# Performance work log

Measured on AMD Instinct MI355X. Metric: run time of the kernel, lower is better.

Reference implementation:

```python
import jax, jax.numpy as jnp
import numpy as np

BEV = 100  # fixed 100x100 BEV grid from __init__


def _bev_grids():
    # x: arange(-25+0.125, 25, 0.5) -> 100 vals; z: arange(0.125, 50, 0.5) -> 100 vals
    x = jnp.arange(-25.0 + 0.125, 25.0, 0.5, dtype=jnp.float32)
    z = jnp.arange(0.125, 50.0, 0.5, dtype=jnp.float32)
    zz, xx = jnp.meshgrid(z, x, indexing='ij')           # [100,100]
    xz = xx / zz                                          # [100,100]
    yz = jnp.stack([-1.0 / zz, 0.5 / zz, 2.0 / zz], 0)    # [3,100,100], planes y=-1,0.5,2
    return xz, yz


def _grid_sample_bilinear(img, grid):
    """torch.nn.functional.grid_sample, mode='bilinear', padding_mode='zeros',
    align_corners=False. img [B,C,H,W], grid [B,Hg,Wg,2] in [-1,1] (u=x, v=y)."""
    B, C, H, W = img.shape
    x = ((grid[..., 0] + 1.0) * W - 1.0) * 0.5            # unnormalized pixel x
    y = ((grid[..., 1] + 1.0) * H - 1.0) * 0.5
    x0f = jnp.floor(x)
    y0f = jnp.floor(y)
    x0 = x0f.astype(jnp.int32)
    y0 = y0f.astype(jnp.int32)
    x1 = x0 + 1
    y1 = y0 + 1
    wx1 = x - x0f
    wx0 = 1.0 - wx1
    wy1 = y - y0f
    wy0 = 1.0 - wy1

    def corner(xi, yi, w):
        valid = ((xi >= 0) & (xi < W) & (yi >= 0) & (yi < H)).astype(img.dtype)
        xi_c = jnp.clip(xi, 0, W - 1)
        yi_c = jnp.clip(yi, 0, H - 1)
        # per-batch gather: [C,H,W] indexed by [Hg,Wg] -> [C,Hg,Wg]
        vals = jax.vmap(lambda im, yy, xx_: im[:, yy, xx_])(img, yi_c, xi_c)
        return vals * (w * valid)[:, None]                 # [B,C,Hg,Wg]

    return (corner(x0, y0, wx0 * wy0) + corner(x1, y0, wx1 * wy0)
            + corner(x0, y1, wx0 * wy1) + corner(x1, y1, wx1 * wy1))


def setup_inputs() -> dict:
    key = jax.random.key(0)
    k1, k2, k3, k4, k5 = jax.random.split(key, 5)
    B, C, H, W = 8, 512, 88, 176
    img_w, img_h = 704, 352
    img_feature = jax.random.normal(k1, (B, C, H, W), dtype=jnp.float32)
    # realistic pinhole intrinsics so many BEV cells project in-bounds
    fx = jax.random.uniform(k2, (B,), minval=450.0, maxval=650.0)
    fy = jax.random.uniform(k3, (B,), minval=450.0, maxval=650.0)
    cx = img_w / 2.0 + jax.random.uniform(k4, (B,), minval=-8.0, maxval=8.0)
    cy = img_h / 2.0 + jax.random.uniform(k5, (B,), minval=-8.0, maxval=8.0)
    intrinsic = (jnp.zeros((B, 3, 3), dtype=jnp.float32)
                 .at[:, 0, 0].set(fx).at[:, 1, 1].set(fy)
                 .at[:, 0, 2].set(cx).at[:, 1, 2].set(cy)
                 .at[:, 2, 2].set(1.0))
    return {"img_feature": img_feature, "intrinsic": intrinsic,
            "img_w": img_w, "img_h": img_h}


def reference(img_feature, intrinsic, img_w, img_h):
    xz, yz = _bev_grids()
    fx = intrinsic[:, 0, 0][:, None, None]
    cx = intrinsic[:, 0, 2][:, None, None]
    fy = intrinsic[:, 1, 1][:, None, None]
    cy = intrinsic[:, 1, 2][:, None, None]
    u = ((fx * xz[None] + cx) / img_w - 0.5) * 2.0        # [B,100,100], shared by all 3 planes
    acc = None
    for k in range(3):                                     # 3 fixed height planes
        v = ((fy * yz[k][None] + cy) / img_h - 0.5) * 2.0
        grid = jnp.stack((u, v), axis=3)                   # [B,100,100,2]
        s = _grid_sample_bilinear(img_feature, grid)       # [B,C,100,100]
        acc = s if acc is None else acc + s
    return acc / 3.0
```

## Files before the change

kernel.cpp:

```cpp
#include <hip/hip_runtime.h>

#define BEVN 100
#define NB 8
#define NC 512
#define FH 88
#define FW 176
#define HWSZ (FH * FW)
#define NG4  (HWSZ / 4)
#define G4PR (FW / 4)
#define NPAIR (BEVN * BEVN / 2)

typedef float    f32x4 __attribute__((ext_vector_type(4)));
typedef float    f32x2 __attribute__((ext_vector_type(2)));
typedef unsigned u32x4 __attribute__((ext_vector_type(4)));

__device__ __forceinline__ unsigned bf16rne(float f) {
    const unsigned b = __float_as_uint(f);
    return (b + 0x7fffu + ((b >> 16) & 1u)) >> 16;
}
__device__ __forceinline__ float lo16f(unsigned u) { return __uint_as_float(u << 16); }
__device__ __forceinline__ float hi16f(unsigned u) { return __uint_as_float(u & 0xffff0000u); }

__global__ __launch_bounds__(1024, 8)
void vt_kernel(const float* __restrict__ img,
               const float* __restrict__ intr,
               const int* __restrict__ p_imw,
               const int* __restrict__ p_imh,
               float* __restrict__ out)
{
    __shared__ unsigned      buf[HWSZ];
    __shared__ float4        ytab[BEVN * 3];
    __shared__ unsigned char marked[FH];

    const int blk = blockIdx.x;
    const int b   = blk >> 8;
    const int bc0 = b * NC + (blk & 255) * 2;
    const int tid = (int)threadIdx.x;

    const float fx  = intr[b * 9 + 0];
    const float cxv = intr[b * 9 + 2];
    const float fy  = intr[b * 9 + 4];
    const float cyv = intr[b * 9 + 5];
    const float wsc = (float)FW / (float)p_imw[0];
    const float hsc = (float)FH / (float)p_imh[0];

    if (tid < FH) marked[tid] = 0;
    __syncthreads();

    if (tid < BEVN * 3) {
        const int   i  = tid / 3;
        const int   k  = tid - 3 * i;
        const float z  = 0.125f + 0.5f * (float)i;
        const float iz = 1.0f / z;
        const float yk = (k == 0) ? -1.0f : ((k == 1) ? 0.5f : 2.0f);
        const float yp = fmaf(fy * yk * iz + cyv, hsc, -0.5f);
        const float yf = floorf(yp);
        const int   y0 = (int)yf;
        float wy1 = yp - yf;
        float wy0 = 1.0f - wy1;
        wy0 = ((unsigned)y0 < (unsigned)FH) ? wy0 : 0.0f;
        wy1 = ((unsigned)(y0 + 1) < (unsigned)FH) ? wy1 : 0.0f;
        if (wy0 != 0.0f) marked[y0] = 1;
        if (wy1 != 0.0f) marked[y0 + 1] = 1;
        const int yb0 = min(max(y0, 0), FH - 1) * FW;
        const int yb1 = min(max(y0 + 1, 0), FH - 1) * FW;
        float4 e;
        e.x = wy0 * (1.0f / 3.0f);
        e.y = wy1 * (1.0f / 3.0f);
        e.z = __int_as_float(yb0);
        e.w = __int_as_float(yb1);
        ytab[tid] = e;
    }
    __syncthreads();

    {
        f32x4* s0 = (f32x4*)(img + (size_t)bc0 * HWSZ);
        f32x4* s1 = s0 + NG4;
        u32x4* l4 = (u32x4*)buf;
        #pragma unroll
        for (int t = 0; t < 4; ++t) {
            const int g = tid + t * 1024;
            if (g < NG4) {
                u32x4 u = {0u, 0u, 0u, 0u};
                const int row = g / G4PR;
                if (marked[row]) {
                    const f32x4 a  = __builtin_nontemporal_load(s0 + g);
                    const f32x4 bb = __builtin_nontemporal_load(s1 + g);
                    u.x = bf16rne(a.x) | (bf16rne(bb.x) << 16);
                    u.y = bf16rne(a.y) | (bf16rne(bb.y) << 16);
                    u.z = bf16rne(a.z) | (bf16rne(bb.z) << 16);
                    u.w = bf16rne(a.w) | (bf16rne(bb.w) << 16);
                }
                l4[g] = u;
            }
        }
    }
    __syncthreads();

    const float axs = 0.5f * fx * wsc;
    const float axb = -24.875f * fx * wsc;
    const float bx  = fmaf(cxv, wsc, -0.5f);

    float* __restrict__ op0 = out + (size_t)bc0 * (BEVN * BEVN);
    float* __restrict__ op1 = op0 + (BEVN * BEVN);

    for (int p = tid; p < NPAIR; p += 1024) {
        const int i  = p / 50;
        const int jp = p - 50 * i;
        const float z    = fmaf(0.5f, (float)i, 0.125f);
        const float invz = __builtin_amdgcn_rcpf(z);

        int   xb[2];
        float w0[2], w1[2];
        #pragma unroll
        for (int e = 0; e < 2; ++e) {
            const float aj   = fmaf((float)(2 * jp + e), axs, axb);
            const float xpix = fmaf(aj, invz, bx);
            const float f    = floorf(xpix);
            const int   x0   = (int)f;
            float wx1 = xpix - f;
            float wx0 = 1.0f - wx1;
            wx0 = ((unsigned)x0 < (unsigned)FW) ? wx0 : 0.0f;
            wx1 = ((unsigned)(x0 + 1) < (unsigned)FW) ? wx1 : 0.0f;
            const int xbe = min(max(x0, 0), FW - 2);
            const int d   = x0 - xbe;
            w0[e] = (d == 0) ? wx0 : ((d < 0) ? wx1 : 0.0f);
            w1[e] = (d == 0) ? wx1 : ((d < 0) ? 0.0f : wx0);
            xb[e] = xbe;
        }

        f32x2 rA, rB;
        const float wsum = (w0[0] + w1[0]) + (w0[1] + w1[1]);
        if (wsum == 0.0f) {
            rA = (f32x2){0.0f, 0.0f};
            rB = (f32x2){0.0f, 0.0f};
        } else {
            float accA[2] = {0.0f, 0.0f};
            float accB[2] = {0.0f, 0.0f};
            #pragma unroll
            for (int k = 0; k < 3; ++k) {
                const float4 e4  = ytab[i * 3 + k];
                const int    yb0 = __float_as_int(e4.z);
                const int    yb1 = __float_as_int(e4.w);
                #pragma unroll
                for (int e = 0; e < 2; ++e) {
                    const unsigned* r0 = buf + (yb0 + xb[e]);
                    const unsigned* r1 = buf + (yb1 + xb[e]);
                    const unsigned u00 = r0[0], u01 = r0[1];
                    const unsigned u10 = r1[0], u11 = r1[1];
                    const float h0a = fmaf(w1[e], lo16f(u01), w0[e] * lo16f(u00));
                    const float h1a = fmaf(w1[e], lo16f(u11), w0[e] * lo16f(u10));
                    accA[e] = fmaf(e4.x, h0a, accA[e]);
                    accA[e] = fmaf(e4.y, h1a, accA[e]);
                    const float h0b = fmaf(w1[e], hi16f(u01), w0[e] * hi16f(u00));
                    const float h1b = fmaf(w1[e], hi16f(u11), w0[e] * hi16f(u10));
                    accB[e] = fmaf(e4.x, h0b, accB[e]);
                    accB[e] = fmaf(e4.y, h1b, accB[e]);
                }
            }
            rA = (f32x2){accA[0], accA[1]};
            rB = (f32x2){accB[0], accB[1]};
        }
        __builtin_nontemporal_store(rA, (f32x2*)(op0 + 2 * p));
        __builtin_nontemporal_store(rB, (f32x2*)(op1 + 2 * p));
    }
}

extern "C" void kernel_launch(void* const* d_in, const int* in_sizes, int n_in,
                              void* d_out, int out_size, void* d_ws, size_t ws_size,
                              hipStream_t stream) {
    const float* img  = (const float*)d_in[0];
    const float* intr = (const float*)d_in[1];
    const int*   imw  = (const int*)d_in[2];
    const int*   imh  = (const int*)d_in[3];
    float*       out  = (float*)d_out;

    dim3 grid(NB * NC / 2);
    dim3 block(1024);
    hipLaunchKernelGGL(vt_kernel, grid, block, 0, stream,
                       img, intr, imw, imh, out);
}
```

Baseline: 82.15 us.

## Split feature staging into two phases overlapping row loads with far-BEV compute

Feature rows are split by which BEV depth half needs them. Rows needed by the far half (i>=50) are staged first. The loads for rows used only by the near half are issued before the far-half compute, so their latency overlaps it, and they are converted and written to LDS afterward. The change also skips whole BEV rows that have no valid vertical sample and skips plane contributions with zero y weight. It adds a serial single-thread list build, an extra barrier and more register pressure from the held prefetch.

```diff
diff --git a/kernel.cpp b/kernel.cpp
--- a/kernel.cpp
+++ b/kernel.cpp
@@ -9,6 +9,7 @@
 #define NG4  (HWSZ / 4)
 #define G4PR (FW / 4)
 #define NPAIR (BEVN * BEVN / 2)
+#define PSPLIT 2500
 
 typedef float    f32x4 __attribute__((ext_vector_type(4)));
 typedef float    f32x2 __attribute__((ext_vector_type(2)));
@@ -30,7 +31,11 @@
 {
     __shared__ unsigned      buf[HWSZ];
     __shared__ float4        ytab[BEVN * 3];
-    __shared__ unsigned char marked[FH];
+    __shared__ unsigned char markA[FH];
+    __shared__ unsigned char markB[FH];
+    __shared__ unsigned char rowlive[BEVN];
+    __shared__ short         listB[FH];
+    __shared__ int           ngB_sh;
 
     const int blk = blockIdx.x;
     const int b   = blk >> 8;
@@ -44,7 +49,8 @@
     const float wsc = (float)FW / (float)p_imw[0];
     const float hsc = (float)FH / (float)p_imh[0];
 
-    if (tid < FH) marked[tid] = 0;
+    if (tid < FH) { markA[tid] = 0; markB[tid] = 0; }
+    if (tid < BEVN) rowlive[tid] = 0;
     __syncthreads();
 
     if (tid < BEVN * 3) {
@@ -60,8 +66,10 @@
         float wy0 = 1.0f - wy1;
         wy0 = ((unsigned)y0 < (unsigned)FH) ? wy0 : 0.0f;
         wy1 = ((unsigned)(y0 + 1) < (unsigned)FH) ? wy1 : 0.0f;
-        if (wy0 != 0.0f) marked[y0] = 1;
-        if (wy1 != 0.0f) marked[y0 + 1] = 1;
+        unsigned char* mk = (i >= 50) ? markA : markB;
+        if (wy0 != 0.0f) mk[y0] = 1;
+        if (wy1 != 0.0f) mk[y0 + 1] = 1;
+        if (wy0 != 0.0f || wy1 != 0.0f) rowlive[i] = 1;
         const int yb0 = min(max(y0, 0), FH - 1) * FW;
         const int yb1 = min(max(y0 + 1, 0), FH - 1) * FW;
         float4 e;
@@ -73,29 +81,46 @@
     }
     __syncthreads();
 
-    {
-        f32x4* s0 = (f32x4*)(img + (size_t)bc0 * HWSZ);
-        f32x4* s1 = s0 + NG4;
-        u32x4* l4 = (u32x4*)buf;
-        #pragma unroll
-        for (int t = 0; t < 4; ++t) {
-            const int g = tid + t * 1024;
-            if (g < NG4) {
-                u32x4 u = {0u, 0u, 0u, 0u};
-                const int row = g / G4PR;
-                if (marked[row]) {
-                    const f32x4 a  = __builtin_nontemporal_load(s0 + g);
-                    const f32x4 bb = __builtin_nontemporal_load(s1 + g);
-                    u.x = bf16rne(a.x) | (bf16rne(bb.x) << 16);
-                    u.y = bf16rne(a.y) | (bf16rne(bb.y) << 16);
-                    u.z = bf16rne(a.z) | (bf16rne(bb.z) << 16);
-                    u.w = bf16rne(a.w) | (bf16rne(bb.w) << 16);
-                }
-                l4[g] = u;
+    if (tid == 0) {
+        int n = 0;
+        for (int r = 0; r < FH; ++r)
+            if (markB[r] && !markA[r]) listB[n++] = (short)r;
+        ngB_sh = n * G4PR;
+    }
+
+    const f32x4* __restrict__ s0 = (const f32x4*)(img + (size_t)bc0 * HWSZ);
+    const f32x4* __restrict__ s1 = s0 + NG4;
+    u32x4* l4 = (u32x4*)buf;
+
+    #pragma unroll
+    for (int t = 0; t < 4; ++t) {
+        const int g = tid + t * 1024;
+        if (g < NG4) {
+            u32x4 u = {0u, 0u, 0u, 0u};
+            const int row = g / G4PR;
+            if (markA[row]) {
+                const f32x4 a  = __builtin_nontemporal_load(s0 + g);
+                const f32x4 bb = __builtin_nontemporal_load(s1 + g);
+                u.x = bf16rne(a.x) | (bf16rne(bb.x) << 16);
+                u.y = bf16rne(a.y) | (bf16rne(bb.y) << 16);
+                u.z = bf16rne(a.z) | (bf16rne(bb.z) << 16);
+                u.w = bf16rne(a.w) | (bf16rne(bb.w) << 16);
             }
+            l4[g] = u;
         }
     }
     __syncthreads();
+    const int ngB = ngB_sh;
+
+    f32x4 ra0, rb0;
+    int   g0 = -1;
+    if (tid < ngB) {
+        const int r = tid / G4PR;
+        const int c = tid - r * G4PR;
+        g0  = (int)listB[r] * G4PR + c;
+        ra0 = __builtin_nontemporal_load(s0 + g0);
+        rb0 = __builtin_nontemporal_load(s1 + g0);
+    }
 
     const float axs = 0.5f * fx * wsc;
     const float axb = -24.875f * fx * wsc;
@@ -104,66 +129,104 @@
     float* __restrict__ op0 = out + (size_t)bc0 * (BEVN * BEVN);
     float* __restrict__ op1 = op0 + (BEVN * BEVN);
 
-    for (int p = tid; p < NPAIR; p += 1024) {
-        const int i  = p / 50;
-        const int jp = p - 50 * i;
-        const float z    = fmaf(0.5f, (float)i, 0.125f);
-        const float invz = __builtin_amdgcn_rcpf(z);
-
-        int   xb[2];
-        float w0[2], w1[2];
-        #pragma unroll
-        for (int e = 0; e < 2; ++e) {
-            const float aj   = fmaf((float)(2 * jp + e), axs, axb);
-            const float xpix = fmaf(aj, invz, bx);
-            const float f    = floorf(xpix);
-            const int   x0   = (int)f;
-            float wx1 = xpix - f;
-            float wx0 = 1.0f - wx1;
-            wx0 = ((unsigned)x0 < (unsigned)FW) ? wx0 : 0.0f;
-            wx1 = ((unsigned)(x0 + 1) < (unsigned)FW) ? wx1 : 0.0f;
-            const int xbe = min(max(x0, 0), FW - 2);
-            const int d   = x0 - xbe;
-            w0[e] = (d == 0) ? wx0 : ((d < 0) ? wx1 : 0.0f);
-            w1[e] = (d == 0) ? wx1 : ((d < 0) ? 0.0f : wx0);
-            xb[e] = xbe;
-        }
-
-        f32x2 rA, rB;
-        const float wsum = (w0[0] + w1[0]) + (w0[1] + w1[1]);
-        if (wsum == 0.0f) {
-            rA = (f32x2){0.0f, 0.0f};
-            rB = (f32x2){0.0f, 0.0f};
-        } else {
-            float accA[2] = {0.0f, 0.0f};
-            float accB[2] = {0.0f, 0.0f};
-            #pragma unroll
-            for (int k = 0; k < 3; ++k) {
-                const float4 e4  = ytab[i * 3 + k];
-                const int    yb0 = __float_as_int(e4.z);
-                const int    yb1 = __float_as_int(e4.w);
-                #pragma unroll
-                for (int e = 0; e < 2; ++e) {
-                    const unsigned* r0 = buf + (yb0 + xb[e]);
-                    const unsigned* r1 = buf + (yb1 + xb[e]);
-                    const unsigned u00 = r0[0], u01 = r0[1];
-                    const unsigned u10 = r1[0], u11 = r1[1];
-                    const float h0a = fmaf(w1[e], lo16f(u01), w0[e] * lo16f(u00));
-                    const float h1a = fmaf(w1[e], lo16f(u11), w0[e] * lo16f(u10));
-                    accA[e] = fmaf(e4.x, h0a, accA[e]);
-                    accA[e] = fmaf(e4.y, h1a, accA[e]);
-                    const float h0b = fmaf(w1[e], hi16f(u01), w0[e] * hi16f(u00));
-                    const float h1b = fmaf(w1[e], hi16f(u11), w0[e] * hi16f(u10));
-                    accB[e] = fmaf(e4.x, h0b, accB[e]);
-                    accB[e] = fmaf(e4.y, h1b, accB[e]);
-                }
-            }
-            rA = (f32x2){accA[0], accA[1]};
-            rB = (f32x2){accB[0], accB[1]};
-        }
-        __builtin_nontemporal_store(rA, (f32x2*)(op0 + 2 * p));
-        __builtin_nontemporal_store(rB, (f32x2*)(op1 + 2 * p));
-    }
+#define PAIR_BODY(p)                                                          \
+    {                                                                         \
+        const int i  = (p) / 50;                                              \
+        const int jp = (p) - 50 * i;                                          \
+        if (!rowlive[i]) {                                                    \
+            const f32x2 zz = {0.0f, 0.0f};                                    \
+            __builtin_nontemporal_store(zz, (f32x2*)(op0 + 2 * (p)));         \
+            __builtin_nontemporal_store(zz, (f32x2*)(op1 + 2 * (p)));         \
+        } else {                                                              \
+            const float z    = fmaf(0.5f, (float)i, 0.125f);                  \
+            const float invz = __builtin_amdgcn_rcpf(z);                      \
+            int   xb[2];                                                      \
+            float w0[2], w1[2];                                               \
+            _Pragma("unroll")                                                 \
+            for (int e = 0; e < 2; ++e) {                                     \
+                const float aj   = fmaf((float)(2 * jp + e), axs, axb);       \
+                const float xpix = fmaf(aj, invz, bx);                        \
+                const float f    = floorf(xpix);                              \
+                const int   x0   = (int)f;                                    \
+                float wx1 = xpix - f;                                         \
+                float wx0 = 1.0f - wx1;                                       \
+                wx0 = ((unsigned)x0 < (unsigned)FW) ? wx0 : 0.0f;             \
+                wx1 = ((unsigned)(x0 + 1) < (unsigned)FW) ? wx1 : 0.0f;       \
+                const int xbe = min(max(x0, 0), FW - 2);                      \
+                const int d   = x0 - xbe;                                     \
+                w0[e] = (d == 0) ? wx0 : ((d < 0) ? wx1 : 0.0f);              \
+                w1[e] = (d == 0) ? wx1 : ((d < 0) ? 0.0f : wx0);              \
+                xb[e] = xbe;                                                  \
+            }                                                                 \
+            f32x2 rA, rB;                                                     \
+            const float wsum = (w0[0] + w1[0]) + (w0[1] + w1[1]);             \
+            if (wsum == 0.0f) {                                               \
+                rA = (f32x2){0.0f, 0.0f};                                     \
+                rB = (f32x2){0.0f, 0.0f};                                     \
+            } else {                                                          \
+                float accA[2] = {0.0f, 0.0f};                                 \
+                float accB[2] = {0.0f, 0.0f};                                 \
+                _Pragma("unroll")                                             \
+                for (int k = 0; k < 3; ++k) {                                 \
+                    const float4 e4 = ytab[i * 3 + k];                        \
+                    if (e4.x != 0.0f || e4.y != 0.0f) {                       \
+                        const int yb0 = __float_as_int(e4.z);                 \
+                        const int yb1 = __float_as_int(e4.w);                 \
+                        _Pragma("unroll")                                     \
+                        for (int e = 0; e < 2; ++e) {                         \
+                            const unsigned* r0 = buf + (yb0 + xb[e]);         \
+                            const unsigned* r1 = buf + (yb1 + xb[e]);         \
+                            const unsigned u00 = r0[0], u01 = r0[1];          \
+                            const unsigned u10 = r1[0], u11 = r1[1];          \
+                            const float h0a = fmaf(w1[e], lo16f(u01), w0[e] * lo16f(u00)); \
+                            const float h1a = fmaf(w1[e], lo16f(u11), w0[e] * lo16f(u10)); \
+                            accA[e] = fmaf(e4.x, h0a, accA[e]);               \
+                            accA[e] = fmaf(e4.y, h1a, accA[e]);               \
+                            const float h0b = fmaf(w1[e], hi16f(u01), w0[e] * hi16f(u00)); \
+                            const float h1b = fmaf(w1[e], hi16f(u11), w0[e] * hi16f(u10)); \
+                            accB[e] = fmaf(e4.x, h0b, accB[e]);               \
+                            accB[e] = fmaf(e4.y, h1b, accB[e]);               \
+                        }                                                     \
+                    }                                                         \
+                }                                                             \
+                rA = (f32x2){accA[0], accA[1]};                               \
+                rB = (f32x2){accB[0], accB[1]};                               \
+            }                                                                 \
+            __builtin_nontemporal_store(rA, (f32x2*)(op0 + 2 * (p)));         \
+            __builtin_nontemporal_store(rB, (f32x2*)(op1 + 2 * (p)));         \
+        }                                                                     \
+    }
+
+    for (int p = PSPLIT + tid; p < NPAIR; p += 1024)
+        PAIR_BODY(p)
+
+    if (g0 >= 0) {
+        u32x4 u;
+        u.x = bf16rne(ra0.x) | (bf16rne(rb0.x) << 16);
+        u.y = bf16rne(ra0.y) | (bf16rne(rb0.y) << 16);
+        u.z = bf16rne(ra0.z) | (bf16rne(rb0.z) << 16);
+        u.w = bf16rne(ra0.w) | (bf16rne(rb0.w) << 16);
+        l4[g0] = u;
+    }
+    for (int idx = tid + 1024; idx < ngB; idx += 1024) {
+        const int r = idx / G4PR;
+        const int c = idx - r * G4PR;
+        const int g = (int)listB[r] * G4PR + c;
+        const f32x4 a  = __builtin_nontemporal_load(s0 + g);
+        const f32x4 bb = __builtin_nontemporal_load(s1 + g);
+        u32x4 u;
+        u.x = bf16rne(a.x) | (bf16rne(bb.x) << 16);
+        u.y = bf16rne(a.y) | (bf16rne(bb.y) << 16);
+        u.z = bf16rne(a.z) | (bf16rne(bb.z) << 16);
+        u.w = bf16rne(a.w) | (bf16rne(bb.w) << 16);
+        l4[g] = u;
+    }
+    __syncthreads();
+
+    for (int p = tid; p < PSPLIT; p += 1024)
+        PAIR_BODY(p)
+
+#undef PAIR_BODY
 }
 
 extern "C" void kernel_launch(void* const* d_in, const int* in_sizes, int n_in,
```

Result: slower. 105.3 us (+28.2%).
